# Performance work log

Measured on AMD Instinct MI355X. Metric: run time of the kernel, lower is better.

Reference implementation:

```python
import jax, jax.numpy as jnp
import numpy as np

H = 128  # hidden width


def _mlp(xy, W0, b0, W1, b1, W2, b2, W3, b3):
    # xy: [..., 2] -> [..., 1], tanh MLP
    h = jnp.tanh(xy @ W0 + b0)
    h = jnp.tanh(h @ W1 + b1)
    h = jnp.tanh(h @ W2 + b2)
    return h @ W3 + b3


def setup_inputs() -> dict:
    key = jax.random.key(0)
    ks = jax.random.split(key, 8)
    n_int, n_bd = 262144, 16384
    inp = {
        "xy_int": jax.random.uniform(ks[0], (n_int, 2), dtype=jnp.float32),
        "f": jax.random.normal(ks[1], (n_int, 1), dtype=jnp.float32),
        "xy_bd": jax.random.uniform(ks[2], (n_bd, 2), dtype=jnp.float32),
        "g": jax.random.normal(ks[3], (n_bd, 1), dtype=jnp.float32),
        # Glorot-ish scaled weights
        "W0": jax.random.normal(ks[4], (2, H), dtype=jnp.float32) / np.sqrt(2.0),
        "b0": jnp.zeros((H,), jnp.float32),
        "W1": jax.random.normal(ks[5], (H, H), dtype=jnp.float32) / np.sqrt(H),
        "b1": jnp.zeros((H,), jnp.float32),
        "W2": jax.random.normal(ks[6], (H, H), dtype=jnp.float32) / np.sqrt(H),
        "b2": jnp.zeros((H,), jnp.float32),
        "W3": jax.random.normal(ks[7], (H, 1), dtype=jnp.float32) / np.sqrt(H),
        "b3": jnp.zeros((1,), jnp.float32),
    }
    return inp


def reference(xy_int, f, xy_bd, g, W0, b0, W1, b1, W2, b2, W3, b3):
    params = (W0, b0, W1, b1, W2, b2, W3, b3)
    n_int = xy_int.shape[0]
    n_bd = xy_bd.shape[0]

    # boundary loss: 0.5/n_bd * ||u(xy_bd) - g||^2
    pred_bd = _mlp(xy_bd, *params)
    diff_bd = pred_bd.reshape(-1) - g.reshape(-1)
    loss_bound = 0.5 / n_bd * jnp.sum(diff_bd * diff_bd)

    # interior PDE residual: u_xx + u_yy (Laplacian) per collocation point
    def u_scalar(p):  # p: [2] -> scalar
        return _mlp(p[None, :], *params)[0, 0]

    def lap_point(p):
        return jnp.trace(jax.hessian(u_scalar)(p))  # 2x2 Hessian trace

    pred_f = jax.vmap(lap_point)(xy_int)  # [n_int]
    diff_f = pred_f.reshape(-1) - f.reshape(-1)
    loss_f = 0.5 / n_int * jnp.sum(diff_f * diff_f)

    return (loss_bound, loss_f)
```

## Files before the change

### kernel.cpp

```cpp
#include <hip/hip_runtime.h>

#define HID 128
#define PTS 32
#define KP  136
#define FRAGS_PER_W 2048
#define WS_ELEMS (FRAGS_PER_W * 8)

typedef float v4f __attribute__((ext_vector_type(4)));
typedef short s8v __attribute__((ext_vector_type(8)));

__device__ __forceinline__ unsigned short f2bf(float f) {
    unsigned u = __builtin_bit_cast(unsigned, f);
    u = (u + 0x7FFFu + ((u >> 16) & 1u)) >> 16;
    return (unsigned short)u;
}
__device__ __forceinline__ float bf2f(unsigned short h) {
    unsigned u = ((unsigned)h) << 16;
    return __builtin_bit_cast(float, u);
}

#if __has_builtin(__builtin_amdgcn_cvt_pk_bf16_f32)
typedef __bf16 bf16x2 __attribute__((ext_vector_type(2)));
__device__ __forceinline__ unsigned pk2(float f0, float f1) {
    return __builtin_bit_cast(unsigned, __builtin_amdgcn_cvt_pk_bf16_f32(f0, f1));
}
#else
__device__ __forceinline__ unsigned pk2(float f0, float f1) {
    unsigned u0 = __builtin_bit_cast(unsigned, f0);
    unsigned u1 = __builtin_bit_cast(unsigned, f1);
    u0 += 0x7FFFu + ((u0 >> 16) & 1u);
    u1 += 0x7FFFu + ((u1 >> 16) & 1u);
    return __builtin_amdgcn_perm(u1, u0, 0x07060302u);
}
#endif

__device__ __forceinline__ v4f tanh4(v4f z) {
#if __has_builtin(__builtin_amdgcn_exp2f)
    v4f zz = z * 2.885390081777927f;
    v4f e = { __builtin_amdgcn_exp2f(zz[0]), __builtin_amdgcn_exp2f(zz[1]),
              __builtin_amdgcn_exp2f(zz[2]), __builtin_amdgcn_exp2f(zz[3]) };
#else
    v4f zz = z * 2.0f;
    v4f e = { __expf(zz[0]), __expf(zz[1]), __expf(zz[2]), __expf(zz[3]) };
#endif
    v4f d = e + 1.0f;
    v4f r = { __builtin_amdgcn_rcpf(d[0]), __builtin_amdgcn_rcpf(d[1]),
              __builtin_amdgcn_rcpf(d[2]), __builtin_amdgcn_rcpf(d[3]) };
    return 1.0f - 2.0f * r;
}

__global__ __launch_bounds__(256) void prep_w_kernel(
    const float* __restrict__ W1, const float* __restrict__ W2,
    unsigned short* __restrict__ ws, float* __restrict__ out)
{
    if (blockIdx.x == 0 && threadIdx.x < 2) out[threadIdx.x] = 0.0f;
    const int t = blockIdx.x * 256 + threadIdx.x;
    const int w = t >> 11;
    const int r = t & 2047;
    const int mtg = r >> 8;
    const int ks = (r >> 6) & 3;
    const int lane = r & 63;
    const int m = mtg * 16 + (lane & 15);
    const int kb = ks * 32 + (lane >> 4) * 8;
    const float* W = w ? W2 : W1;
    s8v hv, lv;
    #pragma unroll
    for (int i = 0; i < 8; ++i) {
        float f = W[(kb + i) * HID + m];
        unsigned short hh = f2bf(f);
        hv[i] = (short)hh;
        lv[i] = (short)f2bf(f - bf2f(hh));
    }
    *(s8v*)&ws[((size_t)(w * 2 + 0) * FRAGS_PER_W + r) * 8] = hv;
    *(s8v*)&ws[((size_t)(w * 2 + 1) * FRAGS_PER_W + r) * 8] = lv;
}

__global__ __launch_bounds__(256, 4) void pinn_mfma_kernel(
    const float* __restrict__ xy_int, const float* __restrict__ f_t,
    const float* __restrict__ xy_bd, const float* __restrict__ g_t,
    const float* __restrict__ W0, const float* __restrict__ b0,
    const float* __restrict__ b1, const float* __restrict__ b2,
    const float* __restrict__ W3, const float* __restrict__ b3,
    const unsigned short* __restrict__ ws, float* __restrict__ out,
    int gi, float scale_int, float scale_bd)
{
    extern __shared__ char smem_raw[];
    unsigned short* sBh = (unsigned short*)smem_raw;
    float* sRed = (float*)(sBh + 4 * 32 * KP);

    const bool is_bd = (int)blockIdx.x >= gi;
    const float* __restrict__ xy  = is_bd ? xy_bd : xy_int;
    const float* __restrict__ tgt = is_bd ? g_t : f_t;
    const int rc = is_bd ? 0 : 3;
    const int pbase = (is_bd ? ((int)blockIdx.x - gi) : (int)blockIdx.x) * PTS;

    const int tid   = threadIdx.x;
    const int lane  = tid & 63;
    const int wave  = tid >> 6;
    const int l15   = lane & 15;
    const int quad  = lane >> 4;
    const int mh    = wave & 1;
    const int pt    = wave >> 1;

    {
        const int tj = tid & 31, tp = tid >> 5;
        const int j0 = tj * 4, p0 = tp * 4;
        v4f xv, yv;
        #pragma unroll
        for (int pp = 0; pp < 4; ++pp) {
            const float2 t2 = ((const float2*)xy)[pbase + p0 + pp];
            xv[pp] = t2.x; yv[pp] = t2.y;
        }
        float wx[4], wy[4], bb[4], n2[4];
        #pragma unroll
        for (int jj = 0; jj < 4; ++jj) {
            wx[jj] = W0[j0 + jj];
            wy[jj] = W0[HID + j0 + jj];
            bb[jj] = b0[j0 + jj];
            n2[jj] = -2.0f * fmaf(wx[jj], wx[jj], wy[jj] * wy[jj]);
        }
        v4f chv[4][4];
        #pragma unroll
        for (int jj = 0; jj < 4; ++jj) {
            v4f z = xv * wx[jj] + yv * wy[jj] + bb[jj];
            v4f a = tanh4(z);
            v4f t = 1.0f - a * a;
            chv[0][jj] = a;
            chv[1][jj] = t * wx[jj];
            chv[2][jj] = t * wy[jj];
            chv[3][jj] = (a * t) * n2[jj];
        }
        #pragma unroll
        for (int pp = 0; pp < 4; ++pp)
            #pragma unroll
            for (int c = 0; c < 4; ++c) {
                const int row = (c * 32 + p0 + pp) * KP + j0;
                uint2 h = { pk2(chv[c][0][pp], chv[c][1][pp]),
                            pk2(chv[c][2][pp], chv[c][3][pp]) };
                *(uint2*)&sBh[row] = h;
            }
    }
    __syncthreads();

    #pragma unroll
    for (int L = 0; L < 2; ++L) {
        const unsigned short* wshi = ws + (size_t)L * 2 * WS_ELEMS;
        const unsigned short* wslo = wshi + WS_ELEMS;

        s8v whi[2][4], wlo[2][4];
        #pragma unroll
        for (int mt = 0; mt < 4; ++mt) {
            const int idx = (mh * 4 + mt) * 256 + lane;
            whi[0][mt] = *(const s8v*)&wshi[(size_t)idx * 8];
            wlo[0][mt] = *(const s8v*)&wslo[(size_t)idx * 8];
        }

        v4f acc[4][4];
        #pragma unroll
        for (int mt = 0; mt < 4; ++mt)
            #pragma unroll
            for (int c = 0; c < 4; ++c)
                acc[mt][c] = (v4f){0.0f, 0.0f, 0.0f, 0.0f};

        #pragma unroll
        for (int ks = 0; ks < 4; ++ks) {
            const int cur = ks & 1, nxt = cur ^ 1;
            if (ks < 3) {
                #pragma unroll
                for (int mt = 0; mt < 4; ++mt) {
                    const int idx = (mh * 4 + mt) * 256 + (ks + 1) * 64 + lane;
                    whi[nxt][mt] = *(const s8v*)&wshi[(size_t)idx * 8];
                    wlo[nxt][mt] = *(const s8v*)&wslo[(size_t)idx * 8];
                }
            }
            #pragma unroll
            for (int c = 0; c < 4; ++c) {
                const int rb = ((c * 2 + pt) * 16 + l15) * KP + quad * 8 + ks * 32;
                s8v bh = *(const s8v*)&sBh[rb];
                #pragma unroll
                for (int mt = 0; mt < 4; ++mt)
                    acc[mt][c] = __builtin_amdgcn_mfma_f32_16x16x32_bf16(
                        whi[cur][mt], bh, acc[mt][c], 0, 0, 0);
                #pragma unroll
                for (int mt = 0; mt < 4; ++mt)
                    acc[mt][c] = __builtin_amdgcn_mfma_f32_16x16x32_bf16(
                        wlo[cur][mt], bh, acc[mt][c], 0, 0, 0);
            }
        }
        __syncthreads();

        const float* __restrict__ bptr = (L == 0) ? b1 : b2;
        #pragma unroll
        for (int mt = 0; mt < 4; ++mt) {
            const int jb = (mh * 4 + mt) * 16 + quad * 4;
            const int rowb = (pt * 16 + l15) * KP + jb;
            v4f bb = *(const v4f*)&bptr[jb];
            v4f z = acc[mt][0] + bb;
            v4f a = tanh4(z);
            if (L == 0) {
                v4f t  = 1.0f - a * a;
                v4f zx = acc[mt][1], zy = acc[mt][2], zl = acc[mt][3];
                v4f s2 = zx * zx + zy * zy;
                v4f c1 = t * zx;
                v4f c2 = t * zy;
                v4f c3 = t * zl + (-2.0f) * ((a * t) * s2);
                uint2 h0 = { pk2(a[0], a[1]),  pk2(a[2], a[3])  };
                uint2 h1 = { pk2(c1[0], c1[1]), pk2(c1[2], c1[3]) };
                uint2 h2 = { pk2(c2[0], c2[1]), pk2(c2[2], c2[3]) };
                uint2 h3 = { pk2(c3[0], c3[1]), pk2(c3[2], c3[3]) };
                *(uint2*)&sBh[rowb]               = h0;
                *(uint2*)&sBh[rowb + 32 * KP]     = h1;
                *(uint2*)&sBh[rowb + 2 * 32 * KP] = h2;
                *(uint2*)&sBh[rowb + 3 * 32 * KP] = h3;
            } else if (is_bd) {
                uint2 h0 = { pk2(a[0], a[1]), pk2(a[2], a[3]) };
                *(uint2*)&sBh[rowb] = h0;
            } else {
                v4f t  = 1.0f - a * a;
                v4f zx = acc[mt][1], zy = acc[mt][2], zl = acc[mt][3];
                v4f s2 = zx * zx + zy * zy;
                v4f c3 = t * zl + (-2.0f) * ((a * t) * s2);
                uint2 h3 = { pk2(c3[0], c3[1]), pk2(c3[2], c3[3]) };
                *(uint2*)&sBh[rowb + 3 * 32 * KP] = h3;
            }
        }
        __syncthreads();
    }

    {
        const int p  = tid >> 3;
        const int i  = tid & 7;
        const int k0 = i * 16;
        const int row = (rc * 32 + p) * KP + k0;
        float r = 0.0f;
        #pragma unroll
        for (int h = 0; h < 2; ++h) {
            s8v vh = *(const s8v*)&sBh[row + h * 8];
            #pragma unroll
            for (int t = 0; t < 8; ++t)
                r = fmaf(bf2f((unsigned short)vh[t]), W3[k0 + h * 8 + t], r);
        }
        r += __shfl_xor(r, 1, 64);
        r += __shfl_xor(r, 2, 64);
        r += __shfl_xor(r, 4, 64);
        if (i == 0) {
            float d = r + (is_bd ? b3[0] : 0.0f) - tgt[pbase + p];
            sRed[p] = d * d;
        }
    }
    __syncthreads();
    if (tid == 0) {
        float s = 0.0f;
        #pragma unroll
        for (int p = 0; p < PTS; ++p) s += sRed[p];
        atomicAdd(out + (is_bd ? 0 : 1), s * (is_bd ? scale_bd : scale_int));
    }
}

extern "C" void kernel_launch(void* const* d_in, const int* in_sizes, int n_in,
                              void* d_out, int out_size, void* d_ws, size_t ws_size,
                              hipStream_t stream) {
    const float* xy_int = (const float*)d_in[0];
    const float* f      = (const float*)d_in[1];
    const float* xy_bd  = (const float*)d_in[2];
    const float* g      = (const float*)d_in[3];
    const float* W0 = (const float*)d_in[4];
    const float* b0 = (const float*)d_in[5];
    const float* W1 = (const float*)d_in[6];
    const float* b1 = (const float*)d_in[7];
    const float* W2 = (const float*)d_in[8];
    const float* b2 = (const float*)d_in[9];
    const float* W3 = (const float*)d_in[10];
    const float* b3 = (const float*)d_in[11];
    float* out = (float*)d_out;
    unsigned short* ws = (unsigned short*)d_ws;

    const int n_int = in_sizes[0] / 2;
    const int n_bd  = in_sizes[2] / 2;

    prep_w_kernel<<<16, 256, 0, stream>>>(W1, W2, ws, out);

    const int smem = (4 * 32 * KP) * 2 + PTS * 4;
    const int gi = n_int / PTS;
    const int gb = n_bd / PTS;

    pinn_mfma_kernel<<<gi + gb, 256, smem, stream>>>(
        xy_int, f, xy_bd, g, W0, b0, b1, b2, W3, b3, ws, out,
        gi, 0.5f / (float)n_int, 0.5f / (float)n_bd);
}
```

Measured before the change: 233.0 us.

## Fuse final W3 projection into layer-2 epilogue and batch tanh evaluations

Computes the output projection (W3 dot product) directly from the fp32 layer-2 accumulators in registers and reduces with cross-lane shuffles and a small shared buffer. This removes the bf16 store to LDS, a barrier, the separate readback pass and the serial 32-element reduction on one thread. It also prefetches layer-1 and layer-2 weight fragments earlier so their loads overlap the layer-0 and epilogue work, and batches 16 exp/rcp calls at a time to expose more independent transcendental instructions. Keeping W3 and the extra prefetch buffers live raises register pressure under the 4-blocks-per-CU launch bound.

```diff
diff --git a/kernel.cpp b/kernel.cpp
--- a/kernel.cpp
+++ b/kernel.cpp
@@ -34,19 +34,32 @@
 }
 #endif
 
-__device__ __forceinline__ v4f tanh4(v4f z) {
+__device__ __forceinline__ float expf2x(float x) {
 #if __has_builtin(__builtin_amdgcn_exp2f)
-    v4f zz = z * 2.885390081777927f;
-    v4f e = { __builtin_amdgcn_exp2f(zz[0]), __builtin_amdgcn_exp2f(zz[1]),
-              __builtin_amdgcn_exp2f(zz[2]), __builtin_amdgcn_exp2f(zz[3]) };
+    return __builtin_amdgcn_exp2f(x * 2.885390081777927f);
 #else
-    v4f zz = z * 2.0f;
-    v4f e = { __expf(zz[0]), __expf(zz[1]), __expf(zz[2]), __expf(zz[3]) };
+    return __expf(2.0f * x);
 #endif
-    v4f d = e + 1.0f;
-    v4f r = { __builtin_amdgcn_rcpf(d[0]), __builtin_amdgcn_rcpf(d[1]),
-              __builtin_amdgcn_rcpf(d[2]), __builtin_amdgcn_rcpf(d[3]) };
-    return 1.0f - 2.0f * r;
+}
+
+__device__ __forceinline__ void tanh16(const v4f z[4], v4f a[4]) {
+    v4f e[4];
+    #pragma unroll
+    for (int m = 0; m < 4; ++m)
+        #pragma unroll
+        for (int i = 0; i < 4; ++i)
+            e[m][i] = expf2x(z[m][i]);
+    v4f d[4];
+    #pragma unroll
+    for (int m = 0; m < 4; ++m) d[m] = e[m] + 1.0f;
+    v4f r[4];
+    #pragma unroll
+    for (int m = 0; m < 4; ++m)
+        #pragma unroll
+        for (int i = 0; i < 4; ++i)
+            r[m][i] = __builtin_amdgcn_rcpf(d[m][i]);
+    #pragma unroll
+    for (int m = 0; m < 4; ++m) a[m] = 1.0f - 2.0f * r[m];
 }
 
 __global__ __launch_bounds__(256) void prep_w_kernel(
@@ -86,12 +99,11 @@
 {
     extern __shared__ char smem_raw[];
     unsigned short* sBh = (unsigned short*)smem_raw;
-    float* sRed = (float*)(sBh + 4 * 32 * KP);
+    float* sPart = (float*)(sBh + 4 * 32 * KP);
 
     const bool is_bd = (int)blockIdx.x >= gi;
     const float* __restrict__ xy  = is_bd ? xy_bd : xy_int;
     const float* __restrict__ tgt = is_bd ? g_t : f_t;
-    const int rc = is_bd ? 0 : 3;
     const int pbase = (is_bd ? ((int)blockIdx.x - gi) : (int)blockIdx.x) * PTS;
 
     const int tid   = threadIdx.x;
@@ -102,6 +114,23 @@
     const int mh    = wave & 1;
     const int pt    = wave >> 1;
 
+    const unsigned short* ws1h = ws;
+    const unsigned short* ws1l = ws + WS_ELEMS;
+    const unsigned short* ws2h = ws + 2 * WS_ELEMS;
+    const unsigned short* ws2l = ws + 3 * WS_ELEMS;
+
+    s8v whi[2][4], wlo[2][4];
+    #pragma unroll
+    for (int mt = 0; mt < 4; ++mt) {
+        const int idx = (mh * 4 + mt) * 256 + lane;
+        whi[0][mt] = *(const s8v*)&ws1h[(size_t)idx * 8];
+        wlo[0][mt] = *(const s8v*)&ws1l[(size_t)idx * 8];
+    }
+    v4f w3v[4];
+    #pragma unroll
+    for (int mt = 0; mt < 4; ++mt)
+        w3v[mt] = *(const v4f*)&W3[(mh * 4 + mt) * 16 + quad * 4];
+
     {
         const int tj = tid & 31, tp = tid >> 5;
         const int j0 = tj * 4, p0 = tp * 4;
@@ -119,16 +148,19 @@
             bb[jj] = b0[j0 + jj];
             n2[jj] = -2.0f * fmaf(wx[jj], wx[jj], wy[jj] * wy[jj]);
         }
+        v4f z[4], a[4];
+        #pragma unroll
+        for (int jj = 0; jj < 4; ++jj)
+            z[jj] = xv * wx[jj] + yv * wy[jj] + bb[jj];
+        tanh16(z, a);
         v4f chv[4][4];
         #pragma unroll
         for (int jj = 0; jj < 4; ++jj) {
-            v4f z = xv * wx[jj] + yv * wy[jj] + bb[jj];
-            v4f a = tanh4(z);
-            v4f t = 1.0f - a * a;
-            chv[0][jj] = a;
+            v4f t = 1.0f - a[jj] * a[jj];
+            chv[0][jj] = a[jj];
             chv[1][jj] = t * wx[jj];
             chv[2][jj] = t * wy[jj];
-            chv[3][jj] = (a * t) * n2[jj];
+            chv[3][jj] = (a[jj] * t) * n2[jj];
         }
         #pragma unroll
         for (int pp = 0; pp < 4; ++pp)
@@ -142,26 +174,13 @@
     }
     __syncthreads();
 
-    #pragma unroll
-    for (int L = 0; L < 2; ++L) {
-        const unsigned short* wshi = ws + (size_t)L * 2 * WS_ELEMS;
-        const unsigned short* wslo = wshi + WS_ELEMS;
-
-        s8v whi[2][4], wlo[2][4];
-        #pragma unroll
-        for (int mt = 0; mt < 4; ++mt) {
-            const int idx = (mh * 4 + mt) * 256 + lane;
-            whi[0][mt] = *(const s8v*)&wshi[(size_t)idx * 8];
-            wlo[0][mt] = *(const s8v*)&wslo[(size_t)idx * 8];
-        }
-
-        v4f acc[4][4];
+    v4f acc[4][4];
+    auto gemm = [&](const unsigned short* wsh, const unsigned short* wsl) {
         #pragma unroll
         for (int mt = 0; mt < 4; ++mt)
             #pragma unroll
             for (int c = 0; c < 4; ++c)
                 acc[mt][c] = (v4f){0.0f, 0.0f, 0.0f, 0.0f};
-
         #pragma unroll
         for (int ks = 0; ks < 4; ++ks) {
             const int cur = ks & 1, nxt = cur ^ 1;
@@ -169,8 +188,8 @@
                 #pragma unroll
                 for (int mt = 0; mt < 4; ++mt) {
                     const int idx = (mh * 4 + mt) * 256 + (ks + 1) * 64 + lane;
-                    whi[nxt][mt] = *(const s8v*)&wshi[(size_t)idx * 8];
-                    wlo[nxt][mt] = *(const s8v*)&wslo[(size_t)idx * 8];
+                    whi[nxt][mt] = *(const s8v*)&wsh[(size_t)idx * 8];
+                    wlo[nxt][mt] = *(const s8v*)&wsl[(size_t)idx * 8];
                 }
             }
             #pragma unroll
@@ -187,73 +206,96 @@
                         wlo[cur][mt], bh, acc[mt][c], 0, 0, 0);
             }
         }
-        __syncthreads();
-
-        const float* __restrict__ bptr = (L == 0) ? b1 : b2;
+    };
+
+    gemm(ws1h, ws1l);
+    __syncthreads();
+
+    #pragma unroll
+    for (int mt = 0; mt < 4; ++mt) {
+        const int idx = (mh * 4 + mt) * 256 + lane;
+        whi[0][mt] = *(const s8v*)&ws2h[(size_t)idx * 8];
+        wlo[0][mt] = *(const s8v*)&ws2l[(size_t)idx * 8];
+    }
+
+    {
+        v4f z[4], a[4];
+        #pragma unroll
+        for (int mt = 0; mt < 4; ++mt) {
+            const int jb = (mh * 4 + mt) * 16 + quad * 4;
+            z[mt] = acc[mt][0] + *(const v4f*)&b1[jb];
+        }
+        tanh16(z, a);
         #pragma unroll
         for (int mt = 0; mt < 4; ++mt) {
             const int jb = (mh * 4 + mt) * 16 + quad * 4;
             const int rowb = (pt * 16 + l15) * KP + jb;
-            v4f bb = *(const v4f*)&bptr[jb];
-            v4f z = acc[mt][0] + bb;
-            v4f a = tanh4(z);
-            if (L == 0) {
-                v4f t  = 1.0f - a * a;
+            v4f t  = 1.0f - a[mt] * a[mt];
+            v4f zx = acc[mt][1], zy = acc[mt][2], zl = acc[mt][3];
+            v4f s2 = zx * zx + zy * zy;
+            v4f u  = (-2.0f * a[mt]) * s2 + zl;
+            v4f c1 = t * zx;
+            v4f c2 = t * zy;
+            v4f c3 = t * u;
+            uint2 h0 = { pk2(a[mt][0], a[mt][1]), pk2(a[mt][2], a[mt][3]) };
+            uint2 h1 = { pk2(c1[0], c1[1]), pk2(c1[2], c1[3]) };
+            uint2 h2 = { pk2(c2[0], c2[1]), pk2(c2[2], c2[3]) };
+            uint2 h3 = { pk2(c3[0], c3[1]), pk2(c3[2], c3[3]) };
+            *(uint2*)&sBh[rowb]               = h0;
+            *(uint2*)&sBh[rowb + 32 * KP]     = h1;
+            *(uint2*)&sBh[rowb + 2 * 32 * KP] = h2;
+            *(uint2*)&sBh[rowb + 3 * 32 * KP] = h3;
+        }
+    }
+    __syncthreads();
+
+    gemm(ws2h, ws2l);
+
+    {
+        v4f z[4], a[4];
+        #pragma unroll
+        for (int mt = 0; mt < 4; ++mt) {
+            const int jb = (mh * 4 + mt) * 16 + quad * 4;
+            z[mt] = acc[mt][0] + *(const v4f*)&b2[jb];
+        }
+        tanh16(z, a);
+        float part = 0.0f;
+        if (is_bd) {
+            #pragma unroll
+            for (int mt = 0; mt < 4; ++mt) {
+                v4f pr = a[mt] * w3v[mt];
+                part += (pr[0] + pr[1]) + (pr[2] + pr[3]);
+            }
+        } else {
+            #pragma unroll
+            for (int mt = 0; mt < 4; ++mt) {
+                v4f t  = 1.0f - a[mt] * a[mt];
                 v4f zx = acc[mt][1], zy = acc[mt][2], zl = acc[mt][3];
                 v4f s2 = zx * zx + zy * zy;
-                v4f c1 = t * zx;
-                v4f c2 = t * zy;
-                v4f c3 = t * zl + (-2.0f) * ((a * t) * s2);
-                uint2 h0 = { pk2(a[0], a[1]),  pk2(a[2], a[3])  };
-                uint2 h1 = { pk2(c1[0], c1[1]), pk2(c1[2], c1[3]) };
-                uint2 h2 = { pk2(c2[0], c2[1]), pk2(c2[2], c2[3]) };
-                uint2 h3 = { pk2(c3[0], c3[1]), pk2(c3[2], c3[3]) };
-                *(uint2*)&sBh[rowb]               = h0;
-                *(uint2*)&sBh[rowb + 32 * KP]     = h1;
-                *(uint2*)&sBh[rowb + 2 * 32 * KP] = h2;
-                *(uint2*)&sBh[rowb + 3 * 32 * KP] = h3;
-            } else if (is_bd) {
-                uint2 h0 = { pk2(a[0], a[1]), pk2(a[2], a[3]) };
-                *(uint2*)&sBh[rowb] = h0;
-            } else {
-                v4f t  = 1.0f - a * a;
-                v4f zx = acc[mt][1], zy = acc[mt][2], zl = acc[mt][3];
-                v4f s2 = zx * zx + zy * zy;
-                v4f c3 = t * zl + (-2.0f) * ((a * t) * s2);
-                uint2 h3 = { pk2(c3[0], c3[1]), pk2(c3[2], c3[3]) };
-                *(uint2*)&sBh[rowb + 3 * 32 * KP] = h3;
-            }
-        }
+                v4f u  = (-2.0f * a[mt]) * s2 + zl;
+                v4f pr = (t * u) * w3v[mt];
+                part += (pr[0] + pr[1]) + (pr[2] + pr[3]);
+            }
+        }
+        part += __shfl_xor(part, 16, 64);
+        part += __shfl_xor(part, 32, 64);
+        if (mh == 1 && quad == 0) sPart[pt * 16 + l15] = part;
         __syncthreads();
-    }
-
-    {
-        const int p  = tid >> 3;
-        const int i  = tid & 7;
-        const int k0 = i * 16;
-        const int row = (rc * 32 + p) * KP + k0;
-        float r = 0.0f;
-        #pragma unroll
-        for (int h = 0; h < 2; ++h) {
-            s8v vh = *(const s8v*)&sBh[row + h * 8];
-            #pragma unroll
-            for (int t = 0; t < 8; ++t)
-                r = fmaf(bf2f((unsigned short)vh[t]), W3[k0 + h * 8 + t], r);
-        }
-        r += __shfl_xor(r, 1, 64);
-        r += __shfl_xor(r, 2, 64);
-        r += __shfl_xor(r, 4, 64);
-        if (i == 0) {
-            float d = r + (is_bd ? b3[0] : 0.0f) - tgt[pbase + p];
-            sRed[p] = d * d;
-        }
-    }
-    __syncthreads();
-    if (tid == 0) {
-        float s = 0.0f;
-        #pragma unroll
-        for (int p = 0; p < PTS; ++p) s += sRed[p];
-        atomicAdd(out + (is_bd ? 0 : 1), s * (is_bd ? scale_bd : scale_int));
+        if (mh == 0) {
+            const int p = pt * 16 + l15;
+            float pred = part + sPart[p] + (is_bd ? b3[0] : 0.0f);
+            float d = pred - tgt[pbase + p];
+            float sq = (quad == 0) ? d * d : 0.0f;
+            sq += __shfl_xor(sq, 1, 64);
+            sq += __shfl_xor(sq, 2, 64);
+            sq += __shfl_xor(sq, 4, 64);
+            sq += __shfl_xor(sq, 8, 64);
+            sq += __shfl_xor(sq, 16, 64);
+            sq += __shfl_xor(sq, 32, 64);
+            if (lane == 0)
+                atomicAdd(out + (is_bd ? 0 : 1),
+                          sq * (is_bd ? scale_bd : scale_int));
+        }
     }
 }
 
```

New measurement: 329.3 us. 1.41x slower.
